# Performance work log

Measured on AMD Instinct MI355X. Metric: run time of the kernel, lower is better.

The kernel has to match this reference:

```python
import jax, jax.numpy as jnp
import numpy as np

BITS = 8
EPS = 1e-5
NUM_HEADS = 16


def quantize_weight(w, eps=EPS):
    # per-tensor abs-mean scale, ternary weights in {-1, 0, 1}
    scale = jnp.maximum(jnp.mean(jnp.abs(w)), eps)
    qw = jnp.clip(jnp.round(w / scale), -1.0, 1.0)
    return qw, scale


def bitlinear158_inference(x, qw, scale, bias=None, bits=BITS, eps=EPS):
    # per-token abs-max activation quantization to [-Q, Q-1]
    q = float(2 ** (bits - 1))
    gamma = jnp.maximum(jnp.max(jnp.abs(x), axis=-1, keepdims=True), eps)
    qx = jnp.clip(jnp.round(x * (q / gamma)), -q, q - 1.0)
    out = jnp.einsum('...i,oi->...o', qx, qw)
    out = out * (scale * gamma / q)
    if bias is not None:
        out = out + bias
    return out


def setup_inputs() -> dict:
    rng = jax.random.key(0)
    ks = jax.random.split(rng, 7)
    B, L, E = 4, 2048, 1024
    return {
        'query': jax.random.normal(ks[0], (B, L, E), jnp.float32),
        'key': jax.random.normal(ks[1], (B, L, E), jnp.float32),
        'value': jax.random.normal(ks[2], (B, L, E), jnp.float32),
        'in_proj_weight': jax.random.normal(ks[3], (3 * E, E), jnp.float32) * 0.02,
        'in_proj_bias': jax.random.normal(ks[4], (3 * E,), jnp.float32) * 0.02,
        'out_proj_weight': jax.random.normal(ks[5], (E, E), jnp.float32) * 0.02,
        'out_proj_bias': jax.random.normal(ks[6], (E,), jnp.float32) * 0.02,
    }


def reference(query, key, value, in_proj_weight, in_proj_bias, out_proj_weight, out_proj_bias):
    B, Lq, E = query.shape
    Lk = key.shape[1]
    H = NUM_HEADS
    D = E // H

    # quantize weights as done at __init__ time
    qw, kw, vw = jnp.split(in_proj_weight, 3, axis=0)  # each [E, E]
    qb, kb, vb = jnp.split(in_proj_bias, 3, axis=0)
    q_qw, q_s = quantize_weight(qw)
    k_qw, k_s = quantize_weight(kw)
    v_qw, v_s = quantize_weight(vw)
    o_qw, o_s = quantize_weight(out_proj_weight)

    # quantized projections [B, L, E]
    q = bitlinear158_inference(query, q_qw, q_s, qb)
    k = bitlinear158_inference(key, k_qw, k_s, kb)
    v = bitlinear158_inference(value, v_qw, v_s, vb)

    # [B, H, L, D]
    q = q.reshape(B, Lq, H, D).transpose(0, 2, 1, 3)
    k = k.reshape(B, Lk, H, D).transpose(0, 2, 1, 3)
    v = v.reshape(B, Lk, H, D).transpose(0, 2, 1, 3)

    scores = jnp.einsum('bhqd,bhkd->bhqk', q, k) / jnp.sqrt(jnp.asarray(D, q.dtype))
    attn = jax.nn.softmax(scores, axis=-1)
    ctx = jnp.einsum('bhqk,bhkd->bhqd', attn, v)  # [B, H, Lq, D]
    ctx = ctx.transpose(0, 2, 1, 3).reshape(B, Lq, E)

    out = bitlinear158_inference(ctx, o_qw, o_s, out_proj_bias)
    return out
```

## Files before the change

### kernel.cpp

```cpp
#include <hip/hip_runtime.h>
#include <cstdint>
#include <cstddef>

#define BB 4
#define LL 2048
#define EE 1024
#define HH 16
#define DD 64
#define TT (BB*LL)
#define EPSF 1e-5f

typedef _Float16 half8 __attribute__((ext_vector_type(8)));
typedef _Float16 half4v __attribute__((ext_vector_type(4)));
typedef float floatx4 __attribute__((ext_vector_type(4)));
typedef float floatx16 __attribute__((ext_vector_type(16)));
typedef int intx4 __attribute__((ext_vector_type(4)));
typedef unsigned int uintx4 __attribute__((ext_vector_type(4)));

__device__ __forceinline__ void gl_lds16(const void* g, void* l) {
    __builtin_amdgcn_global_load_lds(
        (const __attribute__((address_space(1))) void*)g,
        (__attribute__((address_space(3))) void*)l, 16, 0, 0);
}

__device__ __forceinline__ uint32_t pk2(float a, float b) {
    union { _Float16 h[2]; uint32_t u; } x;
    x.h[0] = (_Float16)a; x.h[1] = (_Float16)b;
    return x.u;
}

__global__ void k_absum(const float* __restrict__ in_proj,
                        const float* __restrict__ out_proj,
                        double* __restrict__ sums) {
    const int which = blockIdx.y;
    const float* src = (which < 3) ? (in_proj + (size_t)which * EE * EE) : out_proj;
    double loc = 0.0;
    const int n = EE * EE;
    for (int i = blockIdx.x * blockDim.x + threadIdx.x; i < n; i += gridDim.x * blockDim.x)
        loc += (double)fabsf(src[i]);
    #pragma unroll
    for (int off = 32; off > 0; off >>= 1) loc += __shfl_down(loc, off, 64);
    __shared__ double red[4];
    const int lane = threadIdx.x & 63, wv = threadIdx.x >> 6;
    if (lane == 0) red[wv] = loc;
    __syncthreads();
    if (threadIdx.x == 0) {
        double tot = red[0] + red[1] + red[2] + red[3];
        atomicAdd(&sums[which], tot);
    }
}

__global__ void k_quantw(const float* __restrict__ in_proj,
                         const float* __restrict__ out_proj,
                         const double* __restrict__ sums,
                         float* __restrict__ scaleF,
                         int8_t* __restrict__ qw) {
    const int idx = blockIdx.x * blockDim.x + threadIdx.x;
    if (idx < 4) scaleF[idx] = fmaxf((float)(sums[idx] * (1.0 / (EE * EE))), EPSF);
    const int which = idx >> 20;
    const float s = fmaxf((float)(sums[which] * (1.0 / (EE * EE))), EPSF);
    const float w = (which < 3) ? in_proj[idx] : out_proj[idx - 3 * EE * EE];
    float q = rintf(w / s);
    q = fminf(fmaxf(q, -1.f), 1.f);
    qw[idx] = (int8_t)q;
}

__device__ __forceinline__ void gammaq_body(const float* __restrict__ x,
                                            float* __restrict__ g,
                                            int8_t* __restrict__ qx) {
    const int wv = threadIdx.x >> 6, lane = threadIdx.x & 63;
    const int tok = blockIdx.x * 4 + wv;
    const float* xp = x + (size_t)tok * EE;
    float4 v[4];
    #pragma unroll
    for (int i = 0; i < 4; i++) v[i] = *(const float4*)(xp + (lane + 64 * i) * 4);
    float m = 0.f;
    #pragma unroll
    for (int i = 0; i < 4; i++)
        m = fmaxf(m, fmaxf(fmaxf(fabsf(v[i].x), fabsf(v[i].y)),
                           fmaxf(fabsf(v[i].z), fabsf(v[i].w))));
    #pragma unroll
    for (int off = 1; off < 64; off <<= 1) m = fmaxf(m, __shfl_xor(m, off, 64));
    const float gg = fmaxf(m, EPSF);
    const float rg = 128.f / gg;
    int8_t* qp = qx + (size_t)tok * EE;
    #pragma unroll
    for (int i = 0; i < 4; i++) {
        char4 c;
        c.x = (int8_t)(int)fminf(fmaxf(rintf(v[i].x * rg), -128.f), 127.f);
        c.y = (int8_t)(int)fminf(fmaxf(rintf(v[i].y * rg), -128.f), 127.f);
        c.z = (int8_t)(int)fminf(fmaxf(rintf(v[i].z * rg), -128.f), 127.f);
        c.w = (int8_t)(int)fminf(fmaxf(rintf(v[i].w * rg), -128.f), 127.f);
        *(char4*)(qp + (lane + 64 * i) * 4) = c;
    }
    if (lane == 0) g[tok] = gg;
}

__global__ __launch_bounds__(256) void k_gammaq3(const float* __restrict__ q,
                                                 const float* __restrict__ k,
                                                 const float* __restrict__ v,
                                                 float* __restrict__ g,
                                                 int8_t* __restrict__ qx) {
    const int y = blockIdx.y;
    const float* src = (y == 0) ? q : (y == 1) ? k : v;
    gammaq_body(src, g + (size_t)y * TT, qx + (size_t)y * TT * EE);
}

__global__ __launch_bounds__(256) void k_gammaq(const float* __restrict__ x,
                                                float* __restrict__ g,
                                                int8_t* __restrict__ qx) {
    gammaq_body(x, g, qx);
}

__global__ __launch_bounds__(256) void k_bitmm(
    const int8_t* __restrict__ qx_all, const float* __restrict__ gam_all,
    const int8_t* __restrict__ qw_all, const float* __restrict__ scaleF,
    const float* __restrict__ in_proj_b, const float* __restrict__ out_proj_b,
    float* __restrict__ outF, _Float16* __restrict__ outH_all,
    int wbase, float qpre) {
    __shared__ __align__(16) int8_t smem[36864];
    int8_t (*As)[128] = (int8_t(*)[128])smem;
    int8_t (*Bs)[128] = (int8_t(*)[128])(smem + 16384);
    _Float16 (*Vt)[136] = (_Float16(*)[136])smem;
    const int widx = wbase + blockIdx.z;
    const int8_t* qx = qx_all + (size_t)widx * TT * EE;
    const int8_t* qw = qw_all + (size_t)widx * EE * EE;
    const float* gam = gam_all + (size_t)widx * TT;
    const float* bias = (widx < 3) ? (in_proj_b + widx * EE) : out_proj_b;
    _Float16* outH = outH_all + (size_t)widx * TT * EE;
    const float pre = (widx == 0) ? qpre : 1.0f;
    const int tid = threadIdx.x;
    const int wv = tid >> 6, lane = tid & 63;
    const int quad = lane >> 4, l16 = lane & 15;
    const int wm = wv & 1, wn = wv >> 1;
    const int t0 = blockIdx.x * 128, o0 = blockIdx.y * 128;
    const int srow = lane >> 3, schunk = lane & 7;

    intx4 acc[4][4];
    #pragma unroll
    for (int i = 0; i < 4; i++)
        #pragma unroll
        for (int j = 0; j < 4; j++) acc[i][j] = (intx4){0, 0, 0, 0};

    for (int k0 = 0; k0 < EE; k0 += 128) {
        __syncthreads();
        #pragma unroll
        for (int p = 0; p < 4; p++) {
            const int g = wv * 4 + p;
            const int c = schunk ^ srow ^ (g & 7);
            const int row = g * 8 + srow;
            gl_lds16(qx + (size_t)(t0 + row) * EE + k0 + c * 16, &As[g * 8][0]);
            gl_lds16(qw + (size_t)(o0 + row) * EE + k0 + c * 16, &Bs[g * 8][0]);
        }
        __syncthreads();
        #pragma unroll
        for (int kk = 0; kk < 2; kk++) {
            intx4 af[4], bf[4];
            #pragma unroll
            for (int s4 = 0; s4 < 4; s4++) {
                const int mR = (l16 & 7) ^ ((s4 * 2 + (l16 >> 3)) & 7);
                const int ph = ((kk * 4 + quad) ^ mR) * 16;
                af[s4] = *(const intx4*)&As[wm * 64 + s4 * 16 + l16][ph];
                bf[s4] = *(const intx4*)&Bs[wn * 64 + s4 * 16 + l16][ph];
            }
            #pragma unroll
            for (int sm = 0; sm < 4; sm++)
                #pragma unroll
                for (int sn = 0; sn < 4; sn++)
                    acc[sm][sn] = __builtin_amdgcn_mfma_i32_16x16x64_i8(
                        af[sm], bf[sn], acc[sm][sn], 0, 0, 0);
        }
    }

    const float s = scaleF[widx];
    if (widx == 2) {
        __syncthreads();
        #pragma unroll
        for (int sm = 0; sm < 4; sm++) {
            const int tl = wm * 64 + sm * 16 + quad * 4;
            float mr[4];
            #pragma unroll
            for (int r = 0; r < 4; r++) mr[r] = s * gam[t0 + tl + r] * 0.0078125f;
            #pragma unroll
            for (int sn = 0; sn < 4; sn++) {
                const int ol = wn * 64 + sn * 16 + l16;
                const float b = bias[o0 + ol];
                half4v hv;
                #pragma unroll
                for (int r = 0; r < 4; r++)
                    hv[r] = (_Float16)((float)acc[sm][sn][r] * mr[r] + b);
                *(half4v*)&Vt[ol][tl] = hv;
            }
        }
        __syncthreads();
        const int ol2 = tid >> 1, tc0 = (tid & 1) * 64;
        const int og = o0 + ol2, hh = og >> 6, dd = og & 63;
        const int bb = t0 >> 11, l0 = t0 & (LL - 1);
        _Float16* dst = outH + ((size_t)(bb * HH + hh) * DD + dd) * LL + l0 + tc0;
        #pragma unroll
        for (int i = 0; i < 8; i++)
            *(half8*)(dst + i * 8) = *(const half8*)&Vt[ol2][tc0 + i * 8];
        return;
    }
    #pragma unroll
    for (int sm = 0; sm < 4; sm++) {
        #pragma unroll
        for (int r = 0; r < 4; r++) {
            const int t = t0 + wm * 64 + sm * 16 + quad * 4 + r;
            const float mr = s * gam[t] * 0.0078125f;
            const int b_ = t >> 11, l_ = t & (LL - 1);
            #pragma unroll
            for (int sn = 0; sn < 4; sn++) {
                const int o = o0 + wn * 64 + sn * 16 + l16;
                const float val = (float)acc[sm][sn][r] * mr + bias[o];
                if (widx == 3) {
                    outF[(size_t)t * EE + o] = val;
                } else {
                    const int h_ = o >> 6, d_ = o & 63;
                    outH[((size_t)(b_ * HH + h_) * LL + l_) * DD + d_] = (_Float16)(val * pre);
                }
            }
        }
    }
}

__global__ __launch_bounds__(256, 4) void k_attn5(const _Float16* __restrict__ Q,
                                                  const _Float16* __restrict__ K,
                                                  const _Float16* __restrict__ Vt,
                                                  float* __restrict__ ctx) {
    __shared__ __align__(16) _Float16 Ksh[64][64];
    __shared__ __align__(16) _Float16 Vtsh[64][64];
    const int tid = threadIdx.x;
    const int wv = tid >> 6, lane = tid & 63;
    const int l32 = lane & 31, h2 = lane >> 5;
    const int bh = blockIdx.y, b_ = bh >> 4, h_ = bh & 15;
    const int q0 = blockIdx.x * 128 + wv * 32;
    const int srow = lane >> 3, schunk = lane & 7;

    const _Float16* Qb = Q + (size_t)bh * LL * DD;
    const _Float16* Kb = K + (size_t)bh * LL * DD;
    const _Float16* Vtb = Vt + (size_t)bh * DD * LL;

    half8 qf[4];
    #pragma unroll
    for (int ds = 0; ds < 4; ds++)
        qf[ds] = *(const half8*)(Qb + (size_t)(q0 + l32) * DD + ds * 16 + h2 * 8);

    floatx16 acc[2];
    #pragma unroll
    for (int r = 0; r < 16; r++) { acc[0][r] = 0.f; acc[1][r] = 0.f; }
    float lsum = 0.f;

    for (int kt = 0; kt < LL; kt += 64) {
        __syncthreads();
        #pragma unroll
        for (int u = 0; u < 2; u++) {
            const int g = wv * 2 + u;
            const int c = schunk ^ srow ^ (g & 7);
            const int row = g * 8 + srow;
            gl_lds16(Kb + (size_t)(kt + row) * DD + c * 8, &Ksh[g * 8][0]);
            gl_lds16(Vtb + (size_t)row * LL + kt + c * 8, &Vtsh[g * 8][0]);
        }
        __syncthreads();

        half8 pa[4];
        #pragma unroll
        for (int ks = 0; ks < 2; ks++) {
            const int rowK = ks * 32 + l32;
            const int mK = (l32 & 7) ^ ((ks * 4 + (l32 >> 3)) & 7);
            floatx16 sc;
            #pragma unroll
            for (int r = 0; r < 16; r++) sc[r] = 0.f;
            #pragma unroll
            for (int ds = 0; ds < 4; ds++) {
                const half8 kf = *(const half8*)&Ksh[rowK][((2 * ds + h2) ^ mK) * 8];
                sc = __builtin_amdgcn_mfma_f32_32x32x16_f16(kf, qf[ds], sc, 0, 0, 0);
            }
            float p[16];
            #pragma unroll
            for (int r = 0; r < 16; r++) p[r] = __builtin_amdgcn_exp2f(sc[r]);
            #pragma unroll
            for (int r = 0; r < 16; r++) lsum += p[r];
            uint32_t u_[4][2], o_[4][2];
            #pragma unroll
            for (int c4 = 0; c4 < 4; c4++) {
                u_[c4][0] = pk2(p[4 * c4 + 0], p[4 * c4 + 1]);
                u_[c4][1] = pk2(p[4 * c4 + 2], p[4 * c4 + 3]);
                o_[c4][0] = __shfl_xor(u_[c4][0], 32, 64);
                o_[c4][1] = __shfl_xor(u_[c4][1], 32, 64);
            }
            #pragma unroll
            for (int mm = 0; mm < 2; mm++) {
                const uint32_t ua = h2 ? u_[2 * mm + 1][0] : u_[2 * mm][0];
                const uint32_t ub = h2 ? u_[2 * mm + 1][1] : u_[2 * mm][1];
                const uint32_t oa = h2 ? o_[2 * mm + 1][0] : o_[2 * mm][0];
                const uint32_t ob = h2 ? o_[2 * mm + 1][1] : o_[2 * mm][1];
                uintx4 w;
                w[0] = h2 ? oa : ua;  w[1] = h2 ? ob : ub;
                w[2] = h2 ? ua : oa;  w[3] = h2 ? ub : ob;
                union { uintx4 u; half8 h; } cv; cv.u = w;
                pa[ks * 2 + mm] = cv.h;
            }
        }

        #pragma unroll
        for (int kb = 0; kb < 4; kb++) {
            #pragma unroll
            for (int sd = 0; sd < 2; sd++) {
                const int rowV = sd * 32 + l32;
                const int mV = (l32 & 7) ^ ((sd * 4 + (l32 >> 3)) & 7);
                const half8 vf = *(const half8*)&Vtsh[rowV][((2 * kb + h2) ^ mV) * 8];
                acc[sd] = __builtin_amdgcn_mfma_f32_32x32x16_f16(pa[kb], vf, acc[sd], 0, 0, 0);
            }
        }
    }

    lsum += __shfl_xor(lsum, 32, 64);
    const float invl = 1.f / lsum;
    #pragma unroll
    for (int r = 0; r < 16; r++) {
        const int qrow = (r & 3) + 8 * (r >> 2) + 4 * h2;
        const float iv = __shfl(invl, qrow, 64);
        float* cp = ctx + ((size_t)b_ * LL + q0 + qrow) * EE + h_ * DD + l32;
        cp[0]  = acc[0][r] * iv;
        cp[32] = acc[1][r] * iv;
    }
}

extern "C" void kernel_launch(void* const* d_in, const int* in_sizes, int n_in,
                              void* d_out, int out_size, void* d_ws, size_t ws_size,
                              hipStream_t stream) {
    const float* query      = (const float*)d_in[0];
    const float* key        = (const float*)d_in[1];
    const float* value      = (const float*)d_in[2];
    const float* in_proj_w  = (const float*)d_in[3];
    const float* in_proj_b  = (const float*)d_in[4];
    const float* out_proj_w = (const float*)d_in[5];
    const float* out_proj_b = (const float*)d_in[6];
    float* out = (float*)d_out;

    char* ws = (char*)d_ws;
    double*   sums   = (double*)ws;
    float*    scaleF = (float*)(ws + 32);
    float*    gbuf   = (float*)(ws + 256);
    int8_t*   qw8    = (int8_t*)(ws + (size_t)1  * 1024 * 1024);
    int8_t*   qx8    = (int8_t*)(ws + (size_t)8  * 1024 * 1024);
    _Float16* Qh     = (_Float16*)(ws + (size_t)40 * 1024 * 1024);
    _Float16* Kh     = Qh + (size_t)TT * EE;
    _Float16* Vth    = Kh + (size_t)TT * EE;
    float*    ctx    = out;

    const float QPRE = 0.18033688011112042f;

    hipMemsetAsync(sums, 0, 32, stream);
    k_absum<<<dim3(64, 4), 256, 0, stream>>>(in_proj_w, out_proj_w, sums);
    k_quantw<<<(4 * EE * EE) / 256, 256, 0, stream>>>(in_proj_w, out_proj_w, sums, scaleF, qw8);
    k_gammaq3<<<dim3(TT / 4, 3), 256, 0, stream>>>(query, key, value, gbuf, qx8);

    k_bitmm<<<dim3(TT / 128, EE / 128, 3), 256, 0, stream>>>(
        qx8, gbuf, qw8, scaleF, in_proj_b, out_proj_b, nullptr, Qh, 0, QPRE);

    k_attn5<<<dim3(LL / 128, BB * HH), 256, 0, stream>>>(Qh, Kh, Vth, ctx);

    k_gammaq<<<TT / 4, 256, 0, stream>>>(ctx, gbuf + 3 * TT, qx8 + 3 * (size_t)TT * EE);
    k_bitmm<<<dim3(TT / 128, EE / 128, 1), 256, 0, stream>>>(
        qx8, gbuf, qw8, scaleF, in_proj_b, out_proj_b, out, Qh, 3, QPRE);
}
```

Measured before the change: 354.3 us.

## Double-buffer K/V tiles in attention and use permlane32 swap for P repack

The attention kernel now allocates two LDS buffers for K and V^T tiles and prefetches the next tile while computing on the current one, using a single barrier per iteration. The cross-half shuffle used to repack softmax probabilities into MFMA operands is replaced by permlane32_swap, removing ds_bpermute traffic and select instructions. Wave priority is raised around the MFMA blocks. LDS use doubles, which may limit occupancy.

```diff
diff --git a/kernel.cpp b/kernel.cpp
--- a/kernel.cpp
+++ b/kernel.cpp
@@ -16,6 +16,7 @@
 typedef float floatx16 __attribute__((ext_vector_type(16)));
 typedef int intx4 __attribute__((ext_vector_type(4)));
 typedef unsigned int uintx4 __attribute__((ext_vector_type(4)));
+typedef unsigned int uint2v __attribute__((ext_vector_type(2)));
 
 __device__ __forceinline__ void gl_lds16(const void* g, void* l) {
     __builtin_amdgcn_global_load_lds(
@@ -228,8 +229,8 @@
                                                   const _Float16* __restrict__ K,
                                                   const _Float16* __restrict__ Vt,
                                                   float* __restrict__ ctx) {
-    __shared__ __align__(16) _Float16 Ksh[64][64];
-    __shared__ __align__(16) _Float16 Vtsh[64][64];
+    __shared__ __align__(16) _Float16 Ksh[2][64][64];
+    __shared__ __align__(16) _Float16 Vtsh[2][64][64];
     const int tid = threadIdx.x;
     const int wv = tid >> 6, lane = tid & 63;
     const int l32 = lane & 31, h2 = lane >> 5;
@@ -251,17 +252,32 @@
     for (int r = 0; r < 16; r++) { acc[0][r] = 0.f; acc[1][r] = 0.f; }
     float lsum = 0.f;
 
-    for (int kt = 0; kt < LL; kt += 64) {
-        __syncthreads();
+    {
         #pragma unroll
         for (int u = 0; u < 2; u++) {
             const int g = wv * 2 + u;
             const int c = schunk ^ srow ^ (g & 7);
             const int row = g * 8 + srow;
-            gl_lds16(Kb + (size_t)(kt + row) * DD + c * 8, &Ksh[g * 8][0]);
-            gl_lds16(Vtb + (size_t)row * LL + kt + c * 8, &Vtsh[g * 8][0]);
-        }
-        __syncthreads();
+            gl_lds16(Kb + (size_t)row * DD + c * 8, &Ksh[0][g * 8][0]);
+            gl_lds16(Vtb + (size_t)row * LL + c * 8, &Vtsh[0][g * 8][0]);
+        }
+    }
+    __syncthreads();
+
+    for (int kt = 0; kt < LL; kt += 64) {
+        const int cur = (kt >> 6) & 1;
+
+        if (kt + 64 < LL) {
+            const int nkt = kt + 64;
+            #pragma unroll
+            for (int u = 0; u < 2; u++) {
+                const int g = wv * 2 + u;
+                const int c = schunk ^ srow ^ (g & 7);
+                const int row = g * 8 + srow;
+                gl_lds16(Kb + (size_t)(nkt + row) * DD + c * 8, &Ksh[cur ^ 1][g * 8][0]);
+                gl_lds16(Vtb + (size_t)row * LL + nkt + c * 8, &Vtsh[cur ^ 1][g * 8][0]);
+            }
+        }
 
         half8 pa[4];
         #pragma unroll
@@ -271,48 +287,51 @@
             floatx16 sc;
             #pragma unroll
             for (int r = 0; r < 16; r++) sc[r] = 0.f;
+            __builtin_amdgcn_s_setprio(1);
             #pragma unroll
             for (int ds = 0; ds < 4; ds++) {
-                const half8 kf = *(const half8*)&Ksh[rowK][((2 * ds + h2) ^ mK) * 8];
+                const half8 kf = *(const half8*)&Ksh[cur][rowK][((2 * ds + h2) ^ mK) * 8];
                 sc = __builtin_amdgcn_mfma_f32_32x32x16_f16(kf, qf[ds], sc, 0, 0, 0);
             }
+            __builtin_amdgcn_s_setprio(0);
             float p[16];
             #pragma unroll
             for (int r = 0; r < 16; r++) p[r] = __builtin_amdgcn_exp2f(sc[r]);
             #pragma unroll
             for (int r = 0; r < 16; r++) lsum += p[r];
-            uint32_t u_[4][2], o_[4][2];
+            uint32_t u_[4][2];
             #pragma unroll
             for (int c4 = 0; c4 < 4; c4++) {
                 u_[c4][0] = pk2(p[4 * c4 + 0], p[4 * c4 + 1]);
                 u_[c4][1] = pk2(p[4 * c4 + 2], p[4 * c4 + 3]);
-                o_[c4][0] = __shfl_xor(u_[c4][0], 32, 64);
-                o_[c4][1] = __shfl_xor(u_[c4][1], 32, 64);
             }
             #pragma unroll
             for (int mm = 0; mm < 2; mm++) {
-                const uint32_t ua = h2 ? u_[2 * mm + 1][0] : u_[2 * mm][0];
-                const uint32_t ub = h2 ? u_[2 * mm + 1][1] : u_[2 * mm][1];
-                const uint32_t oa = h2 ? o_[2 * mm + 1][0] : o_[2 * mm][0];
-                const uint32_t ob = h2 ? o_[2 * mm + 1][1] : o_[2 * mm][1];
+                uint2v s0 = __builtin_amdgcn_permlane32_swap(
+                    u_[2 * mm][0], u_[2 * mm + 1][0], false, false);
+                uint2v s1 = __builtin_amdgcn_permlane32_swap(
+                    u_[2 * mm][1], u_[2 * mm + 1][1], false, false);
                 uintx4 w;
-                w[0] = h2 ? oa : ua;  w[1] = h2 ? ob : ub;
-                w[2] = h2 ? ua : oa;  w[3] = h2 ? ub : ob;
+                w[0] = s0[0]; w[1] = s1[0]; w[2] = s0[1]; w[3] = s1[1];
                 union { uintx4 u; half8 h; } cv; cv.u = w;
                 pa[ks * 2 + mm] = cv.h;
             }
         }
 
+        __builtin_amdgcn_s_setprio(1);
         #pragma unroll
         for (int kb = 0; kb < 4; kb++) {
             #pragma unroll
             for (int sd = 0; sd < 2; sd++) {
                 const int rowV = sd * 32 + l32;
                 const int mV = (l32 & 7) ^ ((sd * 4 + (l32 >> 3)) & 7);
-                const half8 vf = *(const half8*)&Vtsh[rowV][((2 * kb + h2) ^ mV) * 8];
+                const half8 vf = *(const half8*)&Vtsh[cur][rowV][((2 * kb + h2) ^ mV) * 8];
                 acc[sd] = __builtin_amdgcn_mfma_f32_32x32x16_f16(pa[kb], vf, acc[sd], 0, 0, 0);
             }
         }
+        __builtin_amdgcn_s_setprio(0);
+
+        __syncthreads();
     }
 
     lsum += __shfl_xor(lsum, 32, 64);
```

Result: faster. 343.1 us (-3.2%).
